# Kernel optimization log

Measured on AMD Instinct MI355X. Metric: run time of the kernel, lower is better.

The kernel has to match this reference:

```python
import jax, jax.numpy as jnp
import numpy as np

B, S, D, H = 1024, 64, 1024, 32
HD = D // H  # 32


def make_rpe_map():
    # one-hot map from 225 relative offsets (15x15) to 64x64 (q,k) board pairs
    out = np.zeros((225, 64 * 64), dtype=np.float32)
    for i in range(8):
        for j in range(8):
            for k in range(8):
                for m in range(8):
                    out[15 * (i - k + 7) + (j - m + 7), 64 * (i * 8 + j) + k * 8 + m] = 1
    return out


RPE_MAP = jnp.asarray(make_rpe_map())  # [225, 4096]


def setup_inputs() -> dict:
    key = jax.random.key(0)
    ks = jax.random.split(key, 11)
    s = 0.02
    return {
        "x": jax.random.normal(ks[0], (B, S, D), jnp.float32),
        "q_w": jax.random.normal(ks[1], (D, D), jnp.float32) * s,
        "q_b": jax.random.normal(ks[2], (D,), jnp.float32) * s,
        "k_w": jax.random.normal(ks[3], (D, D), jnp.float32) * s,
        "k_b": jax.random.normal(ks[4], (D,), jnp.float32) * s,
        "v_w": jax.random.normal(ks[5], (D, D), jnp.float32) * s,
        "v_b": jax.random.normal(ks[6], (D,), jnp.float32) * s,
        "out_w": jax.random.normal(ks[7], (D, D), jnp.float32) * s,
        "out_b": jax.random.normal(ks[8], (D,), jnp.float32) * s,
        "rpe_q_w": jax.random.normal(ks[9], (HD * H, 225), jnp.float32) * s,
        "rpe_k_w": jax.random.normal(ks[10], (HD * H, 225), jnp.float32) * s,
    }


def reference(x, q_w, q_b, k_w, k_b, v_w, v_b, out_w, out_b, rpe_q_w, rpe_k_w):
    b, s, _ = x.shape

    def proj(w, bias):
        # torch Linear: y = x @ w.T + b ; then [B,S,H,HD] -> [B,H,S,HD]
        return (x @ w.T + bias).reshape(b, s, H, HD).transpose(0, 2, 1, 3)

    q = proj(q_w, q_b)
    k = proj(k_w, k_b)
    v = proj(v_w, v_b)

    scores = jnp.einsum('bhqd,bhkd->bhqk', q, k)
    bias_q = (rpe_q_w @ RPE_MAP).reshape(HD, H, 64, 64)  # [d,h,q,k]
    scores = scores + jnp.einsum('bhqd,dhqk->bhqk', q, bias_q)
    bias_k = (rpe_k_w @ RPE_MAP).reshape(HD, H, 64, 64)
    scores = scores + jnp.einsum('bhkd,dhqk->bhqk', k, bias_k)
    scores = scores / jnp.sqrt(jnp.asarray(HD, scores.dtype))

    attn = jax.nn.softmax(scores, axis=-1)
    out = jnp.einsum('bhqk,bhkd->bhqd', attn, v)
    out = out.transpose(0, 2, 1, 3).reshape(b, s, D)
    return out @ out_w.T + out_b
```

## Files before the change

### kernel.cpp

```cpp
#include <hip/hip_runtime.h>
#include <hip/hip_bf16.h>

#define AS1 __attribute__((address_space(1)))
#define AS3 __attribute__((address_space(3)))

typedef __attribute__((ext_vector_type(4))) float f32x4;
typedef __attribute__((ext_vector_type(8))) short b16x8;
typedef __attribute__((ext_vector_type(8))) unsigned short u16x8;
typedef unsigned short u16;

static __device__ __forceinline__ u16 f2b(float f) {
  return __builtin_bit_cast(u16, __float2bfloat16(f));
}
static __device__ __forceinline__ float b2f(u16 u) {
  unsigned v = ((unsigned)u) << 16;
  return __builtin_bit_cast(float, v);
}
static __device__ __forceinline__ void gl2lds16(const u16* g, u16* l) {
  __builtin_amdgcn_global_load_lds((const AS1 void*)g, (AS3 void*)l, 16, 0, 0);
}

__global__ void k_cvt(const float* __restrict__ s, u16* __restrict__ d, long n) {
  long i = ((long)blockIdx.x * 256 + threadIdx.x) * 8;
  if (i >= n) return;
  float4 a = *(const float4*)(s + i);
  float4 b = *(const float4*)(s + i + 4);
  u16x8 o;
  o[0] = f2b(a.x); o[1] = f2b(a.y); o[2] = f2b(a.z); o[3] = f2b(a.w);
  o[4] = f2b(b.x); o[5] = f2b(b.y); o[6] = f2b(b.z); o[7] = f2b(b.w);
  *(u16x8*)(d + i) = o;
}

__global__ void k_rpe(const float* __restrict__ rq, const float* __restrict__ rk,
                      u16* __restrict__ oq, u16* __restrict__ ok) {
  int h = blockIdx.y;
  int r = blockIdx.x * 8 + (threadIdx.x >> 5);
  int d = threadIdx.x & 31;
  const float* s = blockIdx.z ? rk : rq;
  u16* o = blockIdx.z ? ok : oq;
  float v = (r < 225) ? s[(d * 32 + h) * 225 + r] : 0.f;
  o[(h * 240 + r) * 32 + d] = f2b(v);
}

template <int MODE>
__global__ __launch_bounds__(512) void k_gemm(
    const u16* __restrict__ A, const u16* __restrict__ Bw,
    const float* __restrict__ b0, const float* __restrict__ b1, const float* __restrict__ b2,
    u16* __restrict__ oq, float* __restrict__ of, int m_base) {
  __shared__ alignas(16) u16 lds[4][16384];
  const int tid = threadIdx.x;
  const int l = tid & 63, w = tid >> 6;
  const int lo = l & 15, hi = l >> 4;
  const int wr = w >> 2, wc = w & 3;

  const int nbx = gridDim.x;
  const int nb = nbx * gridDim.y;
  const int bid = blockIdx.y * nbx + blockIdx.x;
  const int ord = (bid & 7) * (nb >> 3) + (bid >> 3);
  const int tn = (ord % nbx) * 256, tm = m_base + (ord / nbx) * 256;

  const int sl = (tid & 7) ^ ((tid >> 3) & 7);
  const int srow = 2 * (tid >> 3) + (sl >> 2);
  const int scol = (sl & 3) * 8;
  const u16* gA = A + (size_t)(tm + srow) * 1024 + scol;
  const u16* gB = Bw + (size_t)(tn + srow) * 1024 + scol;
  u16* dst = &lds[0][0] + tid * 8;

  const int p7 = (lo >> 1) & 7;
  const int slr = ((lo & 1) * 4 + hi) ^ p7;
  const int aoff = wr * 4096 + (lo >> 1) * 64 + slr * 8;
  const int boff = 8192 + wc * 2048 + (lo >> 1) * 64 + slr * 8;

  f32x4 acc[8][4];
#pragma unroll
  for (int i = 0; i < 8; ++i)
#pragma unroll
    for (int j = 0; j < 4; ++j) acc[i][j] = (f32x4){0.f, 0.f, 0.f, 0.f};

  b16x8 af[8], bf[4];

#define STG_A(t) { const int kc = (t) * 32; u16* d = dst + ((t) & 3) * 16384; \
    gl2lds16(gA + kc, d);  gl2lds16(gA + 131072 + kc, d + 4096); }
#define STG_B(t) { const int kc = (t) * 32; u16* d = dst + ((t) & 3) * 16384; \
    gl2lds16(gB + kc, d + 8192);  gl2lds16(gB + 131072 + kc, d + 12288); }
#define PHA(bi) { const u16* _b = &lds[0][0] + (bi) * 16384; \
    _Pragma("unroll") for (int _i = 0; _i < 4; ++_i) af[_i] = *(const b16x8*)(_b + aoff + _i * 512); \
    _Pragma("unroll") for (int _j = 0; _j < 4; ++_j) bf[_j] = *(const b16x8*)(_b + boff + _j * 512); \
    __builtin_amdgcn_s_barrier(); \
    asm volatile("s_waitcnt lgkmcnt(0)" ::: "memory"); \
    __builtin_amdgcn_sched_barrier(0); \
    __builtin_amdgcn_s_setprio(1); \
    _Pragma("unroll") for (int _i = 0; _i < 4; ++_i) \
    _Pragma("unroll") for (int _j = 0; _j < 4; ++_j) \
      acc[_i][_j] = __builtin_amdgcn_mfma_f32_16x16x32_bf16(af[_i], bf[_j], acc[_i][_j], 0, 0, 0); \
    __builtin_amdgcn_s_setprio(0); \
    __builtin_amdgcn_s_barrier(); }
#define PHB(bi) { const u16* _b = &lds[0][0] + (bi) * 16384; \
    _Pragma("unroll") for (int _i = 4; _i < 8; ++_i) af[_i] = *(const b16x8*)(_b + aoff + _i * 512); \
    __builtin_amdgcn_s_barrier(); \
    asm volatile("s_waitcnt lgkmcnt(0)" ::: "memory"); \
    __builtin_amdgcn_sched_barrier(0); \
    __builtin_amdgcn_s_setprio(1); \
    _Pragma("unroll") for (int _i = 4; _i < 8; ++_i) \
    _Pragma("unroll") for (int _j = 0; _j < 4; ++_j) \
      acc[_i][_j] = __builtin_amdgcn_mfma_f32_16x16x32_bf16(af[_i], bf[_j], acc[_i][_j], 0, 0, 0); \
    __builtin_amdgcn_s_setprio(0); }
#define WV(n) { asm volatile("s_waitcnt vmcnt(" #n ")" ::: "memory"); \
    __builtin_amdgcn_s_barrier(); asm volatile("" ::: "memory"); }

  STG_A(0) STG_B(0) STG_A(1) STG_B(1) STG_A(2) STG_B(2)
  asm volatile("s_waitcnt vmcnt(8)" ::: "memory");
  __builtin_amdgcn_s_barrier();
  asm volatile("" ::: "memory");

#pragma unroll 4
  for (int kt = 0; kt < 28; ++kt) {
    STG_A(kt + 3)
    PHA(kt & 3)
    STG_B(kt + 3)
    PHB(kt & 3)
    WV(8)
  }
  STG_A(31) PHA(0) STG_B(31) PHB(0) WV(8)
  PHA(1) PHB(1) WV(4)
  PHA(2) PHB(2) WV(0)
  PHA(3) PHB(3)
#undef STG_A
#undef STG_B
#undef PHA
#undef PHB
#undef WV

  if (MODE == 0) {
    const size_t G = 67108864;
    const int g = tn >> 10;
    const float* bias = (g == 0) ? b0 : (g == 1) ? b1 : b2;
    const int nn0 = (tn & 1023) + wc * 64;
#pragma unroll
    for (int j = 0; j < 4; ++j) {
      const int nn = nn0 + j * 16 + lo;
      const float bv = bias[nn];
      const int h = nn >> 5, hd = nn & 31;
      if (g < 2) {
#pragma unroll
        for (int i = 0; i < 8; ++i) {
          const int m0 = tm + wr * 128 + i * 16 + hi * 4;
          const int b = m0 >> 6, s0 = m0 & 63;
          const size_t base = (size_t)g * G + ((size_t)(b * 32 + h) * 64 + s0) * 32 + hd;
#pragma unroll
          for (int r = 0; r < 4; ++r) oq[base + (size_t)r * 32] = f2b(acc[i][j][r] + bv);
        }
      } else {
#pragma unroll
        for (int i = 0; i < 8; ++i) {
          const int m0 = tm + wr * 128 + i * 16 + hi * 4;
          const int b = m0 >> 6, s0 = m0 & 63;
          ushort4 pk;
          pk.x = f2b(acc[i][j][0] + bv);
          pk.y = f2b(acc[i][j][1] + bv);
          pk.z = f2b(acc[i][j][2] + bv);
          pk.w = f2b(acc[i][j][3] + bv);
          *(ushort4*)(oq + 2 * G + ((size_t)(b * 32 + h) * 32 + hd) * 64 + s0) = pk;
        }
      }
    }
  } else {
#pragma unroll
    for (int j = 0; j < 4; ++j) {
      const int n = tn + wc * 64 + j * 16 + lo;
      const float bv = b0[n];
#pragma unroll
      for (int i = 0; i < 8; ++i) {
        const int m0 = tm + wr * 128 + i * 16 + hi * 4;
#pragma unroll
        for (int r = 0; r < 4; ++r) of[(size_t)(m0 + r) * 1024 + n] = acc[i][j][r] + bv;
      }
    }
  }
}

__global__ __launch_bounds__(256) void k_attn(
    const u16* __restrict__ qkv, const u16* __restrict__ rq,
    const u16* __restrict__ rk, u16* __restrict__ att) {
  __shared__ alignas(16) u16 board[16 * 240 * 4];
  u16* pl = board;
  const int l = threadIdx.x & 63, w = threadIdx.x >> 6;
  const int lo = l & 15, hi = l >> 4;
  const int b = blockIdx.x, h = blockIdx.y;
  const size_t G = 67108864;
  const u16* qp = qkv + (size_t)(b * 32 + h) * 2048;
  const u16* kp = qkv + G + (size_t)(b * 32 + h) * 2048;
  const u16* vp = qkv + 2 * G + (size_t)(b * 32 + h) * 2048;

  b16x8 qf = *(const b16x8*)(qp + (w * 16 + lo) * 32 + hi * 8);
  b16x8 v00 = *(const b16x8*)(vp + lo * 64 + hi * 8);
  b16x8 v01 = *(const b16x8*)(vp + lo * 64 + 32 + hi * 8);
  b16x8 v10 = *(const b16x8*)(vp + (16 + lo) * 64 + hi * 8);
  b16x8 v11 = *(const b16x8*)(vp + (16 + lo) * 64 + 32 + hi * 8);

  f32x4 s0[4];
#pragma unroll
  for (int kt = 0; kt < 4; ++kt) {
    b16x8 kf = *(const b16x8*)(kp + (kt * 16 + lo) * 32 + hi * 8);
    f32x4 z = (f32x4){0.f, 0.f, 0.f, 0.f};
    s0[kt] = __builtin_amdgcn_mfma_f32_16x16x32_bf16(qf, kf, z, 0, 0, 0);
  }

  const u16* rqh = rq + (size_t)h * 7680;
#pragma unroll
  for (int nt = 0; nt < 15; ++nt) {
    b16x8 rf = *(const b16x8*)(rqh + (nt * 16 + lo) * 32 + hi * 8);
    f32x4 z = (f32x4){0.f, 0.f, 0.f, 0.f};
    f32x4 c = __builtin_amdgcn_mfma_f32_16x16x32_bf16(qf, rf, z, 0, 0, 0);
    ushort4 pk;
    pk.x = f2b(c[0]); pk.y = f2b(c[1]); pk.z = f2b(c[2]); pk.w = f2b(c[3]);
    *(ushort4*)(board + (((w * 4 + hi) * 240 + nt * 16 + lo) << 2)) = pk;
  }
#pragma unroll
  for (int kt = 0; kt < 4; ++kt)
#pragma unroll
    for (int r = 0; r < 4; ++r) {
      int q = w * 16 + hi * 4 + r, k = kt * 16 + lo;
      int rel = 15 * ((q >> 3) - (k >> 3) + 7) + (q & 7) - (k & 7) + 7;
      s0[kt][r] += b2f(board[((w * 4 + hi) * 240 + rel) * 4 + r]);
    }

  b16x8 kfa = *(const b16x8*)(kp + (w * 16 + lo) * 32 + hi * 8);
  const u16* rkh = rk + (size_t)h * 7680;
#pragma unroll
  for (int nt = 0; nt < 15; ++nt) {
    b16x8 rf = *(const b16x8*)(rkh + (nt * 16 + lo) * 32 + hi * 8);
    f32x4 z = (f32x4){0.f, 0.f, 0.f, 0.f};
    f32x4 c = __builtin_amdgcn_mfma_f32_16x16x32_bf16(kfa, rf, z, 0, 0, 0);
    ushort4 pk;
    pk.x = f2b(c[0]); pk.y = f2b(c[1]); pk.z = f2b(c[2]); pk.w = f2b(c[3]);
    *(ushort4*)(board + (((w * 4 + hi) * 240 + nt * 16 + lo) << 2)) = pk;
  }
  __syncthreads();
#pragma unroll
  for (int kt = 0; kt < 4; ++kt)
#pragma unroll
    for (int r = 0; r < 4; ++r) {
      int q = w * 16 + hi * 4 + r, k = kt * 16 + lo;
      int rel = 15 * ((q >> 3) - (k >> 3) + 7) + (q & 7) - (k & 7) + 7;
      s0[kt][r] += b2f(board[((k >> 2) * 240 + rel) * 4 + (k & 3)]);
    }

  const float sc = 0.17677669529663689f;
#pragma unroll
  for (int kt = 0; kt < 4; ++kt) s0[kt] *= sc;
  float p[4][4], rsum[4];
#pragma unroll
  for (int r = 0; r < 4; ++r) {
    float m = s0[0][r];
    m = fmaxf(m, s0[1][r]); m = fmaxf(m, s0[2][r]); m = fmaxf(m, s0[3][r]);
    m = fmaxf(m, __shfl_xor(m, 1));
    m = fmaxf(m, __shfl_xor(m, 2));
    m = fmaxf(m, __shfl_xor(m, 4));
    m = fmaxf(m, __shfl_xor(m, 8));
    float sum = 0.f;
#pragma unroll
    for (int kt = 0; kt < 4; ++kt) {
      float e = __expf(s0[kt][r] - m);
      p[kt][r] = e;
      sum += e;
    }
    sum += __shfl_xor(sum, 1);
    sum += __shfl_xor(sum, 2);
    sum += __shfl_xor(sum, 4);
    sum += __shfl_xor(sum, 8);
    rsum[r] = 1.f / sum;
  }

  __syncthreads();

#pragma unroll
  for (int kt = 0; kt < 4; ++kt)
#pragma unroll
    for (int r = 0; r < 4; ++r) pl[(w * 16 + hi * 4 + r) * 72 + kt * 16 + lo] = f2b(p[kt][r]);

  f32x4 o0 = (f32x4){0.f, 0.f, 0.f, 0.f}, o1 = (f32x4){0.f, 0.f, 0.f, 0.f};
  {
    b16x8 pa0 = *(const b16x8*)(pl + (w * 16 + lo) * 72 + hi * 8);
    b16x8 pa1 = *(const b16x8*)(pl + (w * 16 + lo) * 72 + 32 + hi * 8);
    o0 = __builtin_amdgcn_mfma_f32_16x16x32_bf16(pa0, v00, o0, 0, 0, 0);
    o1 = __builtin_amdgcn_mfma_f32_16x16x32_bf16(pa0, v10, o1, 0, 0, 0);
    o0 = __builtin_amdgcn_mfma_f32_16x16x32_bf16(pa1, v01, o0, 0, 0, 0);
    o1 = __builtin_amdgcn_mfma_f32_16x16x32_bf16(pa1, v11, o1, 0, 0, 0);
  }

#pragma unroll
  for (int r = 0; r < 4; ++r) {
    int q = w * 16 + hi * 4 + r;
    size_t base = (size_t)(b * 64 + q) * 1024 + h * 32;
    att[base + lo] = f2b(o0[r] * rsum[r]);
    att[base + 16 + lo] = f2b(o1[r] * rsum[r]);
  }
}

extern "C" void kernel_launch(void* const* d_in, const int* in_sizes, int n_in,
                              void* d_out, int out_size, void* d_ws, size_t ws_size,
                              hipStream_t stream) {
  const float* x   = (const float*)d_in[0];
  const float* qw  = (const float*)d_in[1];
  const float* qb  = (const float*)d_in[2];
  const float* kw  = (const float*)d_in[3];
  const float* kb  = (const float*)d_in[4];
  const float* vw  = (const float*)d_in[5];
  const float* vb  = (const float*)d_in[6];
  const float* ow  = (const float*)d_in[7];
  const float* ob  = (const float*)d_in[8];
  const float* rqw = (const float*)d_in[9];
  const float* rkw = (const float*)d_in[10];

  if (ws_size < 680460288ULL) return;
  char* p = (char*)d_ws;
  u16* ws_x   = (u16*)p; p += (size_t)65536 * 1024 * 2;
  u16* ws_w   = (u16*)p; p += (size_t)3 * 1024 * 1024 * 2;
  u16* ws_wo  = (u16*)p; p += (size_t)1024 * 1024 * 2;
  u16* ws_rq  = (u16*)p; p += (size_t)32 * 240 * 32 * 2;
  u16* ws_rk  = (u16*)p; p += (size_t)32 * 240 * 32 * 2;
  u16* ws_qkv = (u16*)p; p += (size_t)3 * 67108864 * 2;
  u16* ws_att = (u16*)p; p += (size_t)65536 * 1024 * 2;

  k_cvt<<<32768, 256, 0, stream>>>(x, ws_x, 67108864L);
  k_cvt<<<512, 256, 0, stream>>>(qw, ws_w, 1048576L);
  k_cvt<<<512, 256, 0, stream>>>(kw, ws_w + 1048576, 1048576L);
  k_cvt<<<512, 256, 0, stream>>>(vw, ws_w + 2097152, 1048576L);
  k_cvt<<<512, 256, 0, stream>>>(ow, ws_wo, 1048576L);
  k_rpe<<<dim3(30, 32, 2), 256, 0, stream>>>(rqw, rkw, ws_rq, ws_rk);

  k_gemm<0><<<dim3(12, 128), 512, 0, stream>>>(ws_x, ws_w, qb, kb, vb, ws_qkv, nullptr, 0);
  k_gemm<0><<<dim3(12, 128), 512, 0, stream>>>(ws_x, ws_w, qb, kb, vb, ws_qkv, nullptr, 32768);
  k_attn<<<dim3(1024, 32), 256, 0, stream>>>(ws_qkv, ws_rq, ws_rk, ws_att);
  k_gemm<1><<<dim3(4, 256), 512, 0, stream>>>(ws_att, ws_wo, ob, nullptr, nullptr, nullptr,
                                              (float*)d_out, 0);
}
```

Before: 1.024 ms.

## Transpose score MFMA so each lane owns a query row; swizzle P tile

Swaps the MFMA operands for QK^T so each lane holds one query row across keys. This lets the softmax max and sum be done with two cross-lane shuffles instead of four per row, and it normalises P before the PV MFMA. The RPE bias gather is rewritten with strength-reduced offsets. P is written to a separate XOR-swizzled LDS buffer using packed bf16 conversion, which removes the second __syncthreads. The cost is extra LDS for the separate P buffer, which may reduce occupancy, and the attention kernel is only one part of a pipeline dominated by GEMMs.

```diff
diff --git a/kernel.cpp b/kernel.cpp
--- a/kernel.cpp
+++ b/kernel.cpp
@@ -15,6 +15,11 @@
 static __device__ __forceinline__ float b2f(u16 u) {
   unsigned v = ((unsigned)u) << 16;
   return __builtin_bit_cast(float, v);
+}
+static __device__ __forceinline__ unsigned cvtpk(float a, float b) {
+  unsigned r;
+  asm("v_cvt_pk_bf16_f32 %0, %1, %2" : "=v"(r) : "v"(a), "v"(b));
+  return r;
 }
 static __device__ __forceinline__ void gl2lds16(const u16* g, u16* l) {
   __builtin_amdgcn_global_load_lds((const AS1 void*)g, (AS3 void*)l, 16, 0, 0);
@@ -183,7 +188,7 @@
     const u16* __restrict__ qkv, const u16* __restrict__ rq,
     const u16* __restrict__ rk, u16* __restrict__ att) {
   __shared__ alignas(16) u16 board[16 * 240 * 4];
-  u16* pl = board;
+  __shared__ alignas(16) u16 pl[64 * 72];
   const int l = threadIdx.x & 63, w = threadIdx.x >> 6;
   const int lo = l & 15, hi = l >> 4;
   const int b = blockIdx.x, h = blockIdx.y;
@@ -193,6 +198,7 @@
   const u16* vp = qkv + 2 * G + (size_t)(b * 32 + h) * 2048;
 
   b16x8 qf = *(const b16x8*)(qp + (w * 16 + lo) * 32 + hi * 8);
+  b16x8 kfa = *(const b16x8*)(kp + (w * 16 + lo) * 32 + hi * 8);
   b16x8 v00 = *(const b16x8*)(vp + lo * 64 + hi * 8);
   b16x8 v01 = *(const b16x8*)(vp + lo * 64 + 32 + hi * 8);
   b16x8 v10 = *(const b16x8*)(vp + (16 + lo) * 64 + hi * 8);
@@ -203,7 +209,7 @@
   for (int kt = 0; kt < 4; ++kt) {
     b16x8 kf = *(const b16x8*)(kp + (kt * 16 + lo) * 32 + hi * 8);
     f32x4 z = (f32x4){0.f, 0.f, 0.f, 0.f};
-    s0[kt] = __builtin_amdgcn_mfma_f32_16x16x32_bf16(qf, kf, z, 0, 0, 0);
+    s0[kt] = __builtin_amdgcn_mfma_f32_16x16x32_bf16(kf, qf, z, 0, 0, 0);
   }
 
   const u16* rqh = rq + (size_t)h * 7680;
@@ -216,16 +222,22 @@
     pk.x = f2b(c[0]); pk.y = f2b(c[1]); pk.z = f2b(c[2]); pk.w = f2b(c[3]);
     *(ushort4*)(board + (((w * 4 + hi) * 240 + nt * 16 + lo) << 2)) = pk;
   }
-#pragma unroll
-  for (int kt = 0; kt < 4; ++kt)
-#pragma unroll
-    for (int r = 0; r < 4; ++r) {
-      int q = w * 16 + hi * 4 + r, k = kt * 16 + lo;
-      int rel = 15 * ((q >> 3) - (k >> 3) + 7) + (q & 7) - (k & 7) + 7;
-      s0[kt][r] += b2f(board[((w * 4 + hi) * 240 + rel) * 4 + r]);
-    }
-
-  b16x8 kfa = *(const b16x8*)(kp + (w * 16 + lo) * 32 + hi * 8);
+
+  const int q = w * 16 + lo, qi = q >> 3, qj = q & 7;
+  const int rowq = w * 4 + (lo >> 2);
+  const int eq = lo & 3;
+
+#pragma unroll
+  for (int kt = 0; kt < 4; ++kt) {
+    const int k0 = kt * 16 + hi * 4;
+    const int rel0 = 15 * (qi - (k0 >> 3) + 7) + qj - (k0 & 7) + 7;
+    const u16* g = board + (rowq * 240 + rel0) * 4 + eq;
+    s0[kt][0] += b2f(g[0]);
+    s0[kt][1] += b2f(g[-4]);
+    s0[kt][2] += b2f(g[-8]);
+    s0[kt][3] += b2f(g[-12]);
+  }
+
   const u16* rkh = rk + (size_t)h * 7680;
 #pragma unroll
   for (int nt = 0; nt < 15; ++nt) {
@@ -237,64 +249,67 @@
     *(ushort4*)(board + (((w * 4 + hi) * 240 + nt * 16 + lo) << 2)) = pk;
   }
   __syncthreads();
+
+#pragma unroll
+  for (int kt = 0; kt < 4; ++kt) {
+    const int k0 = kt * 16 + hi * 4;
+    const int rel0 = 15 * (qi - (k0 >> 3) + 7) + qj - (k0 & 7) + 7;
+    const u16* g = board + ((kt * 4 + hi) * 240 + rel0) * 4;
+    s0[kt][0] += b2f(g[0]);
+    s0[kt][1] += b2f(g[-3]);
+    s0[kt][2] += b2f(g[-6]);
+    s0[kt][3] += b2f(g[-9]);
+  }
+
+  const float sc = 0.17677669529663689f;
+#pragma unroll
+  for (int kt = 0; kt < 4; ++kt) s0[kt] *= sc;
+  float m0 = fmaxf(fmaxf(s0[0][0], s0[0][1]), fmaxf(s0[0][2], s0[0][3]));
+  float m1 = fmaxf(fmaxf(s0[1][0], s0[1][1]), fmaxf(s0[1][2], s0[1][3]));
+  float m2 = fmaxf(fmaxf(s0[2][0], s0[2][1]), fmaxf(s0[2][2], s0[2][3]));
+  float m3 = fmaxf(fmaxf(s0[3][0], s0[3][1]), fmaxf(s0[3][2], s0[3][3]));
+  float m = fmaxf(fmaxf(m0, m1), fmaxf(m2, m3));
+  m = fmaxf(m, __shfl_xor(m, 16));
+  m = fmaxf(m, __shfl_xor(m, 32));
+  float p[4][4];
+  float sum = 0.f;
 #pragma unroll
   for (int kt = 0; kt < 4; ++kt)
 #pragma unroll
     for (int r = 0; r < 4; ++r) {
-      int q = w * 16 + hi * 4 + r, k = kt * 16 + lo;
-      int rel = 15 * ((q >> 3) - (k >> 3) + 7) + (q & 7) - (k & 7) + 7;
-      s0[kt][r] += b2f(board[((k >> 2) * 240 + rel) * 4 + (k & 3)]);
-    }
-
-  const float sc = 0.17677669529663689f;
-#pragma unroll
-  for (int kt = 0; kt < 4; ++kt) s0[kt] *= sc;
-  float p[4][4], rsum[4];
-#pragma unroll
-  for (int r = 0; r < 4; ++r) {
-    float m = s0[0][r];
-    m = fmaxf(m, s0[1][r]); m = fmaxf(m, s0[2][r]); m = fmaxf(m, s0[3][r]);
-    m = fmaxf(m, __shfl_xor(m, 1));
-    m = fmaxf(m, __shfl_xor(m, 2));
-    m = fmaxf(m, __shfl_xor(m, 4));
-    m = fmaxf(m, __shfl_xor(m, 8));
-    float sum = 0.f;
-#pragma unroll
-    for (int kt = 0; kt < 4; ++kt) {
       float e = __expf(s0[kt][r] - m);
       p[kt][r] = e;
       sum += e;
     }
-    sum += __shfl_xor(sum, 1);
-    sum += __shfl_xor(sum, 2);
-    sum += __shfl_xor(sum, 4);
-    sum += __shfl_xor(sum, 8);
-    rsum[r] = 1.f / sum;
-  }
-
-  __syncthreads();
-
-#pragma unroll
-  for (int kt = 0; kt < 4; ++kt)
-#pragma unroll
-    for (int r = 0; r < 4; ++r) pl[(w * 16 + hi * 4 + r) * 72 + kt * 16 + lo] = f2b(p[kt][r]);
-
+  sum += __shfl_xor(sum, 16);
+  sum += __shfl_xor(sum, 32);
+  const float inv = 1.f / sum;
+
+  const int key = q & 7;
+  char* plrow = (char*)pl + q * 144;
+#pragma unroll
+  for (int kt = 0; kt < 4; ++kt) {
+    uint2 pk;
+    pk.x = cvtpk(p[kt][0] * inv, p[kt][1] * inv);
+    pk.y = cvtpk(p[kt][2] * inv, p[kt][3] * inv);
+    const int blk = 2 * kt + (hi >> 1);
+    *(uint2*)(plrow + ((blk ^ key) * 16) + (hi & 1) * 8) = pk;
+  }
+
+  b16x8 pa0 = *(const b16x8*)(plrow + ((hi ^ key) * 16));
+  b16x8 pa1 = *(const b16x8*)(plrow + (((4 + hi) ^ key) * 16));
   f32x4 o0 = (f32x4){0.f, 0.f, 0.f, 0.f}, o1 = (f32x4){0.f, 0.f, 0.f, 0.f};
-  {
-    b16x8 pa0 = *(const b16x8*)(pl + (w * 16 + lo) * 72 + hi * 8);
-    b16x8 pa1 = *(const b16x8*)(pl + (w * 16 + lo) * 72 + 32 + hi * 8);
-    o0 = __builtin_amdgcn_mfma_f32_16x16x32_bf16(pa0, v00, o0, 0, 0, 0);
-    o1 = __builtin_amdgcn_mfma_f32_16x16x32_bf16(pa0, v10, o1, 0, 0, 0);
-    o0 = __builtin_amdgcn_mfma_f32_16x16x32_bf16(pa1, v01, o0, 0, 0, 0);
-    o1 = __builtin_amdgcn_mfma_f32_16x16x32_bf16(pa1, v11, o1, 0, 0, 0);
-  }
+  o0 = __builtin_amdgcn_mfma_f32_16x16x32_bf16(pa0, v00, o0, 0, 0, 0);
+  o1 = __builtin_amdgcn_mfma_f32_16x16x32_bf16(pa0, v10, o1, 0, 0, 0);
+  o0 = __builtin_amdgcn_mfma_f32_16x16x32_bf16(pa1, v01, o0, 0, 0, 0);
+  o1 = __builtin_amdgcn_mfma_f32_16x16x32_bf16(pa1, v11, o1, 0, 0, 0);
 
 #pragma unroll
   for (int r = 0; r < 4; ++r) {
-    int q = w * 16 + hi * 4 + r;
-    size_t base = (size_t)(b * 64 + q) * 1024 + h * 32;
-    att[base + lo] = f2b(o0[r] * rsum[r]);
-    att[base + 16 + lo] = f2b(o1[r] * rsum[r]);
+    const int qr = w * 16 + hi * 4 + r;
+    size_t base = (size_t)(b * 64 + qr) * 1024 + h * 32;
+    att[base + lo] = f2b(o0[r]);
+    att[base + 16 + lo] = f2b(o1[r]);
   }
 }
 
```

After: 1.237 ms. +20.9%, slower.

## Skip unneeded RPE-q tiles per wave and simplify bias gather indexing

Applied to the files above, without the earlier changes.

Each wave now computes only the q-side relative-position MFMA tiles that its 16 query rows can reference, instead of all 15. The RPE weight tables are stored in an XOR-swizzled layout with a precomputed per-lane offset. The bias gather loops use closed-form relative offsets with constant strides instead of per-element index arithmetic. The goal is to cut MFMA work, global loads and integer ALU inside the attention kernel, at the cost of a more intricate index mapping that must stay consistent between k_rpe and k_attn.

```diff
diff --git a/kernel.cpp b/kernel.cpp
--- a/kernel.cpp
+++ b/kernel.cpp
@@ -39,7 +39,9 @@
   const float* s = blockIdx.z ? rk : rq;
   u16* o = blockIdx.z ? ok : oq;
   float v = (r < 225) ? s[(d * 32 + h) * 225 + r] : 0.f;
-  o[(h * 240 + r) * 32 + d] = f2b(v);
+  int p = r >> 1;
+  int sl = (((r & 1) << 2) + (d >> 3)) ^ (p & 7);
+  o[h * 7680 + p * 64 + sl * 8 + (d & 7)] = f2b(v);
 }
 
 template <int MODE>
@@ -191,12 +193,17 @@
   const u16* qp = qkv + (size_t)(b * 32 + h) * 2048;
   const u16* kp = qkv + G + (size_t)(b * 32 + h) * 2048;
   const u16* vp = qkv + 2 * G + (size_t)(b * 32 + h) * 2048;
+  const u16* rqh = rq + (size_t)h * 7680;
+  const u16* rkh = rk + (size_t)h * 7680;
+
+  const int slotoff = (lo >> 1) * 64 + (((((lo & 1) << 2) + hi) ^ ((lo >> 1) & 7)) << 3);
 
   b16x8 qf = *(const b16x8*)(qp + (w * 16 + lo) * 32 + hi * 8);
   b16x8 v00 = *(const b16x8*)(vp + lo * 64 + hi * 8);
   b16x8 v01 = *(const b16x8*)(vp + lo * 64 + 32 + hi * 8);
   b16x8 v10 = *(const b16x8*)(vp + (16 + lo) * 64 + hi * 8);
   b16x8 v11 = *(const b16x8*)(vp + (16 + lo) * 64 + 32 + hi * 8);
+  b16x8 kfa = *(const b16x8*)(kp + (w * 16 + lo) * 32 + hi * 8);
 
   f32x4 s0[4];
 #pragma unroll
@@ -206,30 +213,31 @@
     s0[kt] = __builtin_amdgcn_mfma_f32_16x16x32_bf16(qf, kf, z, 0, 0, 0);
   }
 
-  const u16* rqh = rq + (size_t)h * 7680;
+  const int nt0 = (30 * w) >> 4, nt1 = (30 * w + 134) >> 4;
 #pragma unroll
   for (int nt = 0; nt < 15; ++nt) {
-    b16x8 rf = *(const b16x8*)(rqh + (nt * 16 + lo) * 32 + hi * 8);
-    f32x4 z = (f32x4){0.f, 0.f, 0.f, 0.f};
-    f32x4 c = __builtin_amdgcn_mfma_f32_16x16x32_bf16(qf, rf, z, 0, 0, 0);
-    ushort4 pk;
-    pk.x = f2b(c[0]); pk.y = f2b(c[1]); pk.z = f2b(c[2]); pk.w = f2b(c[3]);
-    *(ushort4*)(board + (((w * 4 + hi) * 240 + nt * 16 + lo) << 2)) = pk;
-  }
-#pragma unroll
-  for (int kt = 0; kt < 4; ++kt)
-#pragma unroll
-    for (int r = 0; r < 4; ++r) {
-      int q = w * 16 + hi * 4 + r, k = kt * 16 + lo;
-      int rel = 15 * ((q >> 3) - (k >> 3) + 7) + (q & 7) - (k & 7) + 7;
-      s0[kt][r] += b2f(board[((w * 4 + hi) * 240 + rel) * 4 + r]);
+    if (nt >= nt0 && nt <= nt1) {
+      b16x8 rf = *(const b16x8*)(rqh + nt * 512 + slotoff);
+      f32x4 z = (f32x4){0.f, 0.f, 0.f, 0.f};
+      f32x4 c = __builtin_amdgcn_mfma_f32_16x16x32_bf16(qf, rf, z, 0, 0, 0);
+      ushort4 pk;
+      pk.x = f2b(c[0]); pk.y = f2b(c[1]); pk.z = f2b(c[2]); pk.w = f2b(c[3]);
+      *(ushort4*)(board + (((w * 4 + hi) * 240 + nt * 16 + lo) << 2)) = pk;
     }
-
-  b16x8 kfa = *(const b16x8*)(kp + (w * 16 + lo) * 32 + hi * 8);
-  const u16* rkh = rk + (size_t)h * 7680;
+  }
+#pragma unroll
+  for (int kt = 0; kt < 4; ++kt) {
+    const int rel0 = 15 * (2 * w + (hi >> 1) - 2 * kt - (lo >> 3) + 7) + (hi & 1) * 4 - (lo & 7) + 7;
+    const u16* g = board + (((w * 4 + hi) * 240 + rel0) << 2);
+    s0[kt][0] += b2f(g[0]);
+    s0[kt][1] += b2f(g[5]);
+    s0[kt][2] += b2f(g[10]);
+    s0[kt][3] += b2f(g[15]);
+  }
+
 #pragma unroll
   for (int nt = 0; nt < 15; ++nt) {
-    b16x8 rf = *(const b16x8*)(rkh + (nt * 16 + lo) * 32 + hi * 8);
+    b16x8 rf = *(const b16x8*)(rkh + nt * 512 + slotoff);
     f32x4 z = (f32x4){0.f, 0.f, 0.f, 0.f};
     f32x4 c = __builtin_amdgcn_mfma_f32_16x16x32_bf16(kfa, rf, z, 0, 0, 0);
     ushort4 pk;
@@ -238,13 +246,14 @@
   }
   __syncthreads();
 #pragma unroll
-  for (int kt = 0; kt < 4; ++kt)
-#pragma unroll
-    for (int r = 0; r < 4; ++r) {
-      int q = w * 16 + hi * 4 + r, k = kt * 16 + lo;
-      int rel = 15 * ((q >> 3) - (k >> 3) + 7) + (q & 7) - (k & 7) + 7;
-      s0[kt][r] += b2f(board[((k >> 2) * 240 + rel) * 4 + (k & 3)]);
-    }
+  for (int kt = 0; kt < 4; ++kt) {
+    const int rel0 = 15 * (2 * w + (hi >> 1) - 2 * kt - (lo >> 3) + 7) + (hi & 1) * 4 - (lo & 7) + 7;
+    const u16* g = board + (((kt * 4 + (lo >> 2)) * 240 + rel0) << 2) + (lo & 3);
+    s0[kt][0] += b2f(g[0]);
+    s0[kt][1] += b2f(g[4]);
+    s0[kt][2] += b2f(g[8]);
+    s0[kt][3] += b2f(g[12]);
+  }
 
   const float sc = 0.17677669529663689f;
 #pragma unroll
@@ -318,8 +327,8 @@
   u16* ws_x   = (u16*)p; p += (size_t)65536 * 1024 * 2;
   u16* ws_w   = (u16*)p; p += (size_t)3 * 1024 * 1024 * 2;
   u16* ws_wo  = (u16*)p; p += (size_t)1024 * 1024 * 2;
-  u16* ws_rq  = (u16*)p; p += (size_t)32 * 240 * 32 * 2;
-  u16* ws_rk  = (u16*)p; p += (size_t)32 * 240 * 32 * 2;
+  u16* ws_rq  = (u16*)p; p += (size_t)32 * 7680 * 2;
+  u16* ws_rk  = (u16*)p; p += (size_t)32 * 7680 * 2;
   u16* ws_qkv = (u16*)p; p += (size_t)3 * 67108864 * 2;
   u16* ws_att = (u16*)p; p += (size_t)65536 * 1024 * 2;
 
```

Measured after the change: 1.040 ms, median of 4. About the same (+1.6%).
